# Optimization experiments

Measured on AMD Instinct MI355X. Metric: run time of the kernel, lower is better.

Reference implementation:

```python
import jax, jax.numpy as jnp
import numpy as np

N = 20000      # vertices
KPV = 8        # key points per vertex
M = N * KPV    # total key points
E = 320000     # edges (avg in-degree 16)
KP_DIM = 4
SD = 300       # state_dim
T = 3          # GNN iterations
NC = 4         # classes
LOC = (64, 64, 7)


def _lin(key, din, dout):
    k1, k2 = jax.random.split(key)
    s = 1.0 / np.sqrt(din)
    W = jax.random.uniform(k1, (din, dout), jnp.float32, -s, s)
    b = jax.random.uniform(k2, (dout,), jnp.float32, -s, s)
    return W, b


def setup_inputs():
    key = jax.random.key(0)
    ks = jax.random.split(key, 32)
    inp = {}
    inp['key_points'] = jax.random.normal(ks[0], (M, KP_DIM), jnp.float32)
    inp['pos'] = jax.random.normal(ks[1], (N, 3), jnp.float32)
    # uniform ragged layout: vertex i owns key points [i*KPV, (i+1)*KPV)
    inp['key_points_lookup'] = jnp.arange(N, dtype=jnp.int32) * KPV
    inp['edge_index'] = jax.random.randint(ks[2], (2, E), 0, N, jnp.int32)
    # MLPInit: kp_dim -> 64 -> 128 -> state_dim (basic_block = Linear+ReLU)
    inp['Wi0'], inp['bi0'] = _lin(ks[3], KP_DIM, 64)
    inp['Wi1'], inp['bi1'] = _lin(ks[4], 64, 128)
    inp['Wi2'], inp['bi2'] = _lin(ks[5], 128, SD)
    # MLPInitAggr: state_dim -> state_dim
    inp['Wa'], inp['ba'] = _lin(ks[6], SD, SD)
    # StateConvLayer params per iteration (mlp_h: s->delta_x, mlp_f: [dx,s_j]->e, mlp_g: update)
    Wh, bh, Wf, bf, Wg, bg = [], [], [], [], [], []
    for t in range(T):
        w, b = _lin(ks[7 + 3 * t], SD, 3); Wh.append(w); bh.append(b)
        w, b = _lin(ks[8 + 3 * t], SD + 3, SD); Wf.append(w); bf.append(b)
        w, b = _lin(ks[9 + 3 * t], SD, SD); Wg.append(w); bg.append(b)
    inp['Wh'] = jnp.stack(Wh); inp['bh'] = jnp.stack(bh)
    inp['Wf'] = jnp.stack(Wf); inp['bf'] = jnp.stack(bf)
    inp['Wg'] = jnp.stack(Wg); inp['bg'] = jnp.stack(bg)
    # classification head: state_dim -> 64 -> n_classes
    inp['Wc1'], inp['bc1'] = _lin(ks[16], SD, 64)
    inp['Wc2'], inp['bc2'] = _lin(ks[17], 64, NC)
    # per-class localization heads: state_dim -> 64 -> 64 -> 7 (stacked over classes)
    Wl1, bl1, Wl2, bl2, Wl3, bl3 = [], [], [], [], [], []
    for c in range(NC):
        w, b = _lin(ks[18 + 3 * c], SD, LOC[0]); Wl1.append(w); bl1.append(b)
        w, b = _lin(ks[19 + 3 * c], LOC[0], LOC[1]); Wl2.append(w); bl2.append(b)
        w, b = _lin(ks[20 + 3 * c], LOC[1], LOC[2]); Wl3.append(w); bl3.append(b)
    inp['Wl1'] = jnp.stack(Wl1); inp['bl1'] = jnp.stack(bl1)
    inp['Wl2'] = jnp.stack(Wl2); inp['bl2'] = jnp.stack(bl2)
    inp['Wl3'] = jnp.stack(Wl3); inp['bl3'] = jnp.stack(bl3)
    return inp


def reference(key_points, pos, key_points_lookup, edge_index,
              Wi0, bi0, Wi1, bi1, Wi2, bi2, Wa, ba,
              Wh, bh, Wf, bf, Wg, bg,
              Wc1, bc1, Wc2, bc2,
              Wl1, bl1, Wl2, bl2, Wl3, bl3):
    relu = jax.nn.relu
    n = pos.shape[0]
    # ---- initial vertex state: per-key-point MLP + ragged segment-max ----
    feats = relu(key_points @ Wi0 + bi0)
    feats = relu(feats @ Wi1 + bi1)
    feats = relu(feats @ Wi2 + bi2)                      # [M, SD]
    seg = jnp.searchsorted(key_points_lookup,
                           jnp.arange(feats.shape[0], dtype=jnp.int32),
                           side='right') - 1              # key point -> vertex id
    kp_max = jax.ops.segment_max(feats, seg, num_segments=n)  # [N, SD]
    s = relu(kp_max @ Wa + ba)                            # initial vertex states
    # ---- GNN iterations (Point-GNN eqns, max aggregation) ----
    src, dst = edge_index[0], edge_index[1]
    for t in range(Wh.shape[0]):
        dx = s @ Wh[t] + bh[t]                            # [N, 3] predicted offset
        m = jnp.concatenate([pos[src] - pos[dst] + dx[dst], s[src]], axis=-1)
        e = relu(m @ Wf[t] + bf[t])                       # [E, SD] edge messages
        aggr = jax.ops.segment_max(e, dst, num_segments=n)
        aggr = jnp.where(jnp.isneginf(aggr), 0.0, aggr)   # empty segments -> 0
        s = s + (aggr @ Wg[t] + bg[t])                    # residual state update
    # ---- heads ----
    cls_pred = relu(relu(s @ Wc1 + bc1) @ Wc2 + bc2)      # [N, NC]
    h = relu(jnp.einsum('nd,cdk->cnk', s, Wl1) + bl1[:, None, :])
    h = relu(jnp.einsum('cnd,cdk->cnk', h, Wl2) + bl2[:, None, :])
    h = relu(jnp.einsum('cnd,cdk->cnk', h, Wl3) + bl3[:, None, :])  # [C, N, 7]
    reg_pred = jnp.transpose(h, (1, 0, 2)).reshape(n, -1)           # [N, C*7]
    return cls_pred, reg_pred
```

## Files before the change

kernel.cpp:

```cpp
#include <hip/hip_runtime.h>
#include <stdint.h>

#define N_V   20000
#define M_KP  160000
#define E_N   320000
#define SD    300
#define T_IT  3

typedef unsigned short bf16_t;
typedef __attribute__((ext_vector_type(8))) short short8_t;
typedef __attribute__((ext_vector_type(4))) float float4_t;

__device__ __forceinline__ float bf2f(bf16_t u) {
    return __uint_as_float(((unsigned)u) << 16);
}
__device__ __forceinline__ bf16_t f2bf(float f) {
    unsigned u = __float_as_uint(f);
    unsigned r = (u + 0x7FFFu + ((u >> 16) & 1u)) >> 16;
    return (bf16_t)r;
}

template<bool F32>
__device__ __forceinline__ float LD(const void* p, size_t i) {
    if (F32) return ((const float*)p)[i];
    return bf2f(((const bf16_t*)p)[i]);
}
template<bool F32>
__device__ __forceinline__ void ST(void* p, size_t i, float v) {
    if (F32) ((float*)p)[i] = v;
    else     ((bf16_t*)p)[i] = f2bf(v);
}
__device__ __forceinline__ float LDr(const void* p, long long i, bool f32) {
    return f32 ? ((const float*)p)[i] : bf2f(((const bf16_t*)p)[i]);
}
__device__ __forceinline__ void STr(void* p, size_t i, float v, bool f32) {
    if (f32) ((float*)p)[i] = v;
    else     ((bf16_t*)p)[i] = f2bf(v);
}

__global__ void k_detect(const unsigned* __restrict__ w, int* __restrict__ flag) {
    __shared__ int cnt_s;
    if (threadIdx.x == 0) cnt_s = 0;
    __syncthreads();
    unsigned u = w[threadIdx.x];
    unsigned lo = u & 0xFFFFu;
    int e = (lo >> 7) & 0xFF;
    int plaus = (lo == 0u) || (e >= 96 && e <= 126);
    atomicAdd(&cnt_s, plaus);
    __syncthreads();
    if (threadIdx.x == 0) flag[0] = (cnt_s >= 64) ? 0 : 1;
}

__global__ void k_zero(int* p, int n) {
    int i = blockIdx.x * blockDim.x + threadIdx.x;
    if (i < n) p[i] = 0;
}
__global__ void k_hist(const int* __restrict__ dst, int* __restrict__ cnt) {
    int e = blockIdx.x * blockDim.x + threadIdx.x;
    if (e < E_N) atomicAdd(&cnt[dst[e]], 1);
}
__global__ void k_scan(const int* __restrict__ cnt, int* __restrict__ offs,
                       int* __restrict__ cur) {
    __shared__ int buf[1024];
    __shared__ int carry_s;
    int tid = threadIdx.x;
    if (tid == 0) { carry_s = 0; offs[0] = 0; }
    __syncthreads();
    for (int base = 0; base < N_V; base += 1024) {
        int i = base + tid;
        int v = (i < N_V) ? cnt[i] : 0;
        buf[tid] = v;
        __syncthreads();
        for (int off = 1; off < 1024; off <<= 1) {
            int t = (tid >= off) ? buf[tid - off] : 0;
            __syncthreads();
            buf[tid] += t;
            __syncthreads();
        }
        int incl = buf[tid] + carry_s;
        if (i < N_V) { offs[i + 1] = incl; cur[i] = incl - v; }
        __syncthreads();
        if (tid == 1023) carry_s = incl;
        __syncthreads();
    }
}
__global__ void k_scatter(const int* __restrict__ src, const int* __restrict__ dst,
                          int* __restrict__ cur, int* __restrict__ esrc) {
    int e = blockIdx.x * blockDim.x + threadIdx.x;
    if (e < E_N) {
        int p = atomicAdd(&cur[dst[e]], 1);
        esrc[p] = src[e];
    }
}

template<bool F32>
__global__ __launch_bounds__(256) void k_init_fused(
    const void* __restrict__ kp,
    const void* __restrict__ Wi0, const void* __restrict__ bi0,
    const void* __restrict__ Wi1, const void* __restrict__ bi1,
    const void* __restrict__ Wi2, const void* __restrict__ bi2,
    float* __restrict__ kpmax, const int* __restrict__ flag) {
    if ((flag[0] != 0) != F32) return;
    __shared__ float kps[256];
    __shared__ float h1s[64][64];
    __shared__ float h2s[64 * 128];
    int tid = threadIdx.x;
    int row0 = blockIdx.x * 64;
    kps[tid] = LD<F32>(kp, (size_t)row0 * 4 + tid);
    __syncthreads();
    {
        int c = tid & 63;
        float w0 = LD<F32>(Wi0, c), w1 = LD<F32>(Wi0, 64 + c);
        float w2 = LD<F32>(Wi0, 128 + c), w3 = LD<F32>(Wi0, 192 + c);
        float b0 = LD<F32>(bi0, c);
        int rbase = (tid >> 6) * 16;
#pragma unroll
        for (int rr = 0; rr < 16; rr++) {
            int r = rbase + rr;
            float a = b0 + kps[r * 4] * w0 + kps[r * 4 + 1] * w1
                         + kps[r * 4 + 2] * w2 + kps[r * 4 + 3] * w3;
            h1s[r][c] = fmaxf(a, 0.f);
        }
    }
    __syncthreads();
    {
        int c = tid & 127;
        int rbase = (tid >> 7) * 32;
        float b1 = LD<F32>(bi1, c);
        float acc[32];
#pragma unroll
        for (int rr = 0; rr < 32; rr++) acc[rr] = b1;
        for (int k = 0; k < 64; k++) {
            float wv = LD<F32>(Wi1, (size_t)k * 128 + c);
#pragma unroll
            for (int rr = 0; rr < 32; rr++) acc[rr] += h1s[rbase + rr][k] * wv;
        }
#pragma unroll
        for (int rr = 0; rr < 32; rr++)
            h2s[(size_t)(rbase + rr) * 128 + c] = fmaxf(acc[rr], 0.f);
    }
    __syncthreads();
    {
        int cx = tid & 63, rg = tid >> 6;
        float acc[16][5];
#pragma unroll
        for (int r = 0; r < 16; r++)
#pragma unroll
            for (int j = 0; j < 5; j++) acc[r][j] = 0.f;
        bool ok4 = (cx < SD - 256);
        for (int k = 0; k < 128; k++) {
            float w[5];
#pragma unroll
            for (int j = 0; j < 4; j++) w[j] = LD<F32>(Wi2, (size_t)k * SD + cx + 64 * j);
            w[4] = ok4 ? LD<F32>(Wi2, (size_t)k * SD + cx + 256) : 0.f;
#pragma unroll
            for (int r = 0; r < 16; r++) {
                float av = h2s[(rg * 16 + r) * 128 + k];
#pragma unroll
                for (int j = 0; j < 5; j++) acc[r][j] += av * w[j];
            }
        }
        int vbase = (row0 >> 3) + rg * 2;
#pragma unroll
        for (int half = 0; half < 2; half++) {
            int v = vbase + half;
#pragma unroll
            for (int j = 0; j < 5; j++) {
                int c = cx + 64 * j;
                if (c >= SD) continue;
                float m = acc[half * 8][j];
#pragma unroll
                for (int r = 1; r < 8; r++) m = fmaxf(m, acc[half * 8 + r][j]);
                kpmax[(size_t)v * SD + c] = fmaxf(m + LD<F32>(bi2, c), 0.f);
            }
        }
    }
}

template<bool F32>
__global__ __launch_bounds__(256) void k_gemm(
    const float* __restrict__ A, const void* __restrict__ W,
    const void* __restrict__ bias, const float* res,
    float* C, int Mr, int K, int Nc, int do_relu, const int* __restrict__ flag) {
    if ((flag[0] != 0) != F32) return;
    __shared__ float As[16][65];
    __shared__ float Ws[16][64];
    int tid = threadIdx.x;
    int tx = tid & 15, ty = tid >> 4;
    int row0 = blockIdx.y * 64, col0 = blockIdx.x * 64;
    float acc[4][4] = {{0.f}};
    int lk = tid & 15, lr = tid >> 4;
    int ln = tid & 63, lk4 = tid >> 6;
    for (int k0 = 0; k0 < K; k0 += 16) {
#pragma unroll
        for (int i = 0; i < 4; i++) {
            int r = lr + i * 16;
            int gr = row0 + r, gk = k0 + lk;
            As[lk][r] = (gr < Mr && gk < K) ? A[(size_t)gr * K + gk] : 0.f;
        }
#pragma unroll
        for (int p = 0; p < 4; p++) {
            int kk = lk4 + p * 4;
            int gk = k0 + kk, gn = col0 + ln;
            Ws[kk][ln] = (gk < K && gn < Nc) ? LD<F32>(W, (size_t)gk * Nc + gn) : 0.f;
        }
        __syncthreads();
#pragma unroll
        for (int kk = 0; kk < 16; kk++) {
            float a[4], w[4];
#pragma unroll
            for (int i = 0; i < 4; i++) a[i] = As[kk][ty * 4 + i];
#pragma unroll
            for (int j = 0; j < 4; j++) w[j] = Ws[kk][tx * 4 + j];
#pragma unroll
            for (int i = 0; i < 4; i++)
#pragma unroll
                for (int j = 0; j < 4; j++) acc[i][j] += a[i] * w[j];
        }
        __syncthreads();
    }
#pragma unroll
    for (int i = 0; i < 4; i++) {
        int gr = row0 + ty * 4 + i;
        if (gr >= Mr) continue;
#pragma unroll
        for (int j = 0; j < 4; j++) {
            int gn = col0 + tx * 4 + j;
            if (gn >= Nc) continue;
            float c = acc[i][j] + LD<F32>(bias, gn);
            if (res) c += res[(size_t)gr * Nc + gn];
            if (do_relu) c = fmaxf(c, 0.f);
            C[(size_t)gr * Nc + gn] = c;
        }
    }
}

#define PREP_SPLIT 882688
#define PREP_BIAS  3104
#define PREP_WF3   2700
#define PREP_TOT   (PREP_SPLIT + PREP_BIAS + PREP_WF3 + 32)

__global__ __launch_bounds__(256) void k_prep(
    const void* __restrict__ Wa, const void* __restrict__ Wf,
    const void* __restrict__ Wg, const void* __restrict__ Wc1,
    const void* __restrict__ Wl1, const void* __restrict__ Wl2,
    const void* __restrict__ Wi1, const void* __restrict__ Wi2,
    const void* __restrict__ ba, const void* __restrict__ bfb,
    const void* __restrict__ bgb, const void* __restrict__ bc1,
    const void* __restrict__ bl1b, const void* __restrict__ bl2b,
    const void* __restrict__ bi1, const void* __restrict__ bi2,
    unsigned short* __restrict__ SP, float* __restrict__ biasF,
    float* __restrict__ wf3F,
    float* __restrict__ bzero, const int* __restrict__ flag)
{
    int idx = blockIdx.x * 256 + threadIdx.x;
    if (idx >= PREP_TOT) return;
    bool f32 = flag[0] != 0;
    if (idx < PREP_SPLIT) {
        const void* src; long long eoff, cum; int srcN, Nn, Kk, Kpad, pe, local;
        if (idx < 716800) {
            int m = idx / 102400; local = idx - m * 102400;
            pe = 102400; cum = (long long)m * 102400;
            Kpad = 320; Nn = 300; Kk = 300; srcN = 300;
            src = (m == 0) ? Wa : (m <= 3 ? Wf : Wg);
            eoff = (m == 0) ? 0 : (m <= 3 ? (long long)((m - 1) * 303 + 3) * 300
                                          : (long long)(m - 4) * 90000);
        } else if (idx < 819200) {
            int j = (idx - 716800) / 20480; local = (idx - 716800) - j * 20480;
            pe = 20480; cum = 716800 + (long long)j * 20480;
            Kpad = 320; Nn = 64; Kk = 300; srcN = 64;
            src = (j == 0) ? Wc1 : Wl1;
            eoff = (j == 0) ? 0 : (long long)(j - 1) * 19200;
        } else if (idx < 835584) {
            int c = (idx - 819200) / 4096; local = (idx - 819200) - c * 4096;
            pe = 4096; cum = 819200 + (long long)c * 4096;
            Kpad = 64; Nn = 64; Kk = 64; srcN = 64;
            src = Wl2; eoff = (long long)c * 4096;
        } else if (idx < 843776) {
            local = idx - 835584;
            pe = 8192; cum = 835584;
            Kpad = 64; Nn = 128; Kk = 64; srcN = 128;
            src = Wi1; eoff = 0;
        } else {
            local = idx - 843776;
            pe = 38912; cum = 843776;
            Kpad = 128; Nn = 300; Kk = 128; srcN = 300;
            src = Wi2; eoff = 0;
        }
        int n = local / Kpad, k = local - n * Kpad;
        float v = 0.f;
        if (n < Nn && k < Kk) v = LDr(src, eoff + (long long)k * srcN + n, f32);
        bf16_t hi = f2bf(v);
        bf16_t lo = f2bf(v - bf2f(hi));
        SP[2 * cum + local] = hi;
        SP[2 * cum + pe + local] = lo;
    } else if (idx < PREP_SPLIT + PREP_BIAS) {
        int b = idx - PREP_SPLIT;
        const void* src; int o;
        if (b < 300)       { src = ba;   o = b; }
        else if (b < 1200) { src = bfb;  o = b - 300; }
        else if (b < 2100) { src = bgb;  o = b - 1200; }
        else if (b < 2164) { src = bc1;  o = b - 2100; }
        else if (b < 2420) { src = bl1b; o = b - 2164; }
        else if (b < 2676) { src = bl2b; o = b - 2420; }
        else if (b < 2804) { src = bi1;  o = b - 2676; }
        else               { src = bi2;  o = b - 2804; }
        biasF[b] = LDr(src, o, f32);
    } else if (idx < PREP_SPLIT + PREP_BIAS + PREP_WF3) {
        int b2 = idx - (PREP_SPLIT + PREP_BIAS);
        int t = b2 / 900, rem = b2 - t * 900;
        wf3F[b2] = LDr(Wf, (long long)t * 303 * SD + rem, f32);
    } else {
        bzero[idx - (PREP_SPLIT + PREP_BIAS + PREP_WF3)] = 0.f;
    }
}

__device__ __forceinline__ void mfma16(float4_t& c, short8_t a, short8_t b) {
    asm("v_mfma_f32_16x16x32_bf16 %0, %1, %2, %0" : "+v"(c) : "v"(a), "v"(b));
}
__device__ __forceinline__ void split2(float a, float b, unsigned& h, unsigned& l) {
    asm("v_cvt_pk_bf16_f32 %0, %1, %2" : "=v"(h) : "v"(a), "v"(b));
    float la = a - __uint_as_float(h << 16);
    float lb = b - __uint_as_float(h & 0xFFFF0000u);
    asm("v_cvt_pk_bf16_f32 %0, %1, %2" : "=v"(l) : "v"(la), "v"(lb));
}
__device__ __forceinline__ void split8(float4_t x0, float4_t x1,
                                       short8_t* hi, short8_t* lo) {
    union { unsigned u[4]; short8_t v; } H, L;
#pragma unroll
    for (int p = 0; p < 4; p++) {
        float a, b;
        if (p == 0)      { a = x0[0]; b = x0[1]; }
        else if (p == 1) { a = x0[2]; b = x0[3]; }
        else if (p == 2) { a = x1[0]; b = x1[1]; }
        else             { a = x1[2]; b = x1[3]; }
        unsigned ph, pl;
        split2(a, b, ph, pl);
        H.u[p] = ph; L.u[p] = pl;
    }
    *hi = H.v; *lo = L.v;
}

__global__ __launch_bounds__(256) void k_init_mfma(
    const void* __restrict__ kp,
    const void* __restrict__ Wi0, const void* __restrict__ bi0,
    const unsigned short* __restrict__ W1T,
    const unsigned short* __restrict__ W2T,
    const float* __restrict__ b1F, const float* __restrict__ b2F,
    float* __restrict__ kpmax, const int* __restrict__ flag)
{
    bool f32 = flag[0] != 0;
    __shared__ __attribute__((aligned(16))) unsigned short lds[2][8704];
    int tid = threadIdx.x;
    int w = tid >> 6, lane = tid & 63;
    int rg = w >> 1, ch = w & 1;
    int l15 = lane & 15, g = lane >> 4;
    unsigned short* h2h = lds[rg];
    unsigned short* h2l = lds[rg] + 4352;
    int rw0 = blockIdx.x * 64 + rg * 32;

    float kpr[2][4];
#pragma unroll
    for (int mt = 0; mt < 2; mt++) {
        long long r = rw0 + mt * 16 + l15;
#pragma unroll
        for (int j = 0; j < 4; j++) kpr[mt][j] = LDr(kp, r * 4 + j, f32);
    }
    short8_t a1h[2][2], a1l[2][2];
#pragma unroll
    for (int ks = 0; ks < 2; ks++) {
        float h[2][8];
#pragma unroll
        for (int e = 0; e < 8; e++) {
            int chn = ks * 32 + 8 * g + e;
            float w0 = LDr(Wi0, chn, f32),       w1 = LDr(Wi0, 64 + chn, f32);
            float w2 = LDr(Wi0, 128 + chn, f32), w3 = LDr(Wi0, 192 + chn, f32);
            float b0 = LDr(bi0, chn, f32);
#pragma unroll
            for (int mt = 0; mt < 2; mt++)
                h[mt][e] = fmaxf(b0 + kpr[mt][0] * w0 + kpr[mt][1] * w1
                                    + kpr[mt][2] * w2 + kpr[mt][3] * w3, 0.f);
        }
#pragma unroll
        for (int mt = 0; mt < 2; mt++) {
            union { unsigned u[4]; short8_t v; } H, L;
#pragma unroll
            for (int p = 0; p < 4; p++) {
                unsigned hh, ll;
                split2(h[mt][2 * p], h[mt][2 * p + 1], hh, ll);
                H.u[p] = hh; L.u[p] = ll;
            }
            a1h[mt][ks] = H.v; a1l[mt][ks] = L.v;
        }
    }

#pragma unroll
    for (int i = 0; i < 4; i++) {
        int n0 = ch * 4 + i;
        const unsigned short* bp = W1T + (n0 * 16 + l15) * 64 + 8 * g;
        short8_t bh0 = *(const short8_t*)bp;
        short8_t bh1 = *(const short8_t*)(bp + 32);
        short8_t bl0 = *(const short8_t*)(bp + 8192);
        short8_t bl1 = *(const short8_t*)(bp + 8224);
        float4_t c0 = {0.f, 0.f, 0.f, 0.f}, c1 = {0.f, 0.f, 0.f, 0.f};
        mfma16(c0, a1h[0][0], bh0); mfma16(c0, a1h[0][1], bh1);
        mfma16(c0, a1l[0][0], bh0); mfma16(c0, a1l[0][1], bh1);
        mfma16(c0, a1h[0][0], bl0); mfma16(c0, a1h[0][1], bl1);
        mfma16(c1, a1h[1][0], bh0); mfma16(c1, a1h[1][1], bh1);
        mfma16(c1, a1l[1][0], bh0); mfma16(c1, a1l[1][1], bh1);
        mfma16(c1, a1h[1][0], bl0); mfma16(c1, a1h[1][1], bl1);
        int col = n0 * 16 + l15;
        float bv = b1F[col];
#pragma unroll
        for (int i2 = 0; i2 < 4; i2++) {
            float v0 = fmaxf(c0[i2] + bv, 0.f);
            bf16_t h0 = f2bf(v0);
            h2h[(4 * g + i2) * 136 + col] = h0;
            h2l[(4 * g + i2) * 136 + col] = f2bf(v0 - bf2f(h0));
            float v1 = fmaxf(c1[i2] + bv, 0.f);
            bf16_t h1v = f2bf(v1);
            h2h[(16 + 4 * g + i2) * 136 + col] = h1v;
            h2l[(16 + 4 * g + i2) * 136 + col] = f2bf(v1 - bf2f(h1v));
        }
    }
    __syncthreads();

    short8_t a2h[2][4], a2l[2][4];
#pragma unroll
    for (int mt = 0; mt < 2; mt++)
#pragma unroll
        for (int ks = 0; ks < 4; ks++) {
            int off = (mt * 16 + l15) * 136 + ks * 32 + 8 * g;
            a2h[mt][ks] = *(const short8_t*)(h2h + off);
            a2l[mt][ks] = *(const short8_t*)(h2l + off);
        }
    int vb = blockIdx.x * 8 + rg * 4;
    int n0beg = ch ? 10 : 0, n0end = ch ? 19 : 10;
    for (int n0 = n0beg; n0 < n0end; n0++) {
        const unsigned short* bp = W2T + (n0 * 16 + l15) * 128 + 8 * g;
        short8_t bh[4], bl[4];
#pragma unroll
        for (int ks = 0; ks < 4; ks++) {
            bh[ks] = *(const short8_t*)(bp + ks * 32);
            bl[ks] = *(const short8_t*)(bp + 38912 + ks * 32);
        }
        float4_t c0 = {0.f, 0.f, 0.f, 0.f}, c1 = {0.f, 0.f, 0.f, 0.f};
#pragma unroll
        for (int ks = 0; ks < 4; ks++) {
            mfma16(c0, a2h[0][ks], bh[ks]); mfma16(c1, a2h[1][ks], bh[ks]);
        }
#pragma unroll
        for (int ks = 0; ks < 4; ks++) {
            mfma16(c0, a2l[0][ks], bh[ks]); mfma16(c1, a2l[1][ks], bh[ks]);
        }
#pragma unroll
        for (int ks = 0; ks < 4; ks++) {
            mfma16(c0, a2h[0][ks], bl[ks]); mfma16(c1, a2h[1][ks], bl[ks]);
        }
        float m0 = fmaxf(fmaxf(c0[0], c0[1]), fmaxf(c0[2], c0[3]));
        m0 = fmaxf(m0, __shfl_xor(m0, 16));
        float m1 = fmaxf(fmaxf(c1[0], c1[1]), fmaxf(c1[2], c1[3]));
        m1 = fmaxf(m1, __shfl_xor(m1, 16));
        int col = n0 * 16 + l15;
        if (col < SD) {
            float bv = b2F[col];
            if (g == 0) {
                kpmax[(size_t)(vb + 0) * SD + col] = fmaxf(m0 + bv, 0.f);
                kpmax[(size_t)(vb + 2) * SD + col] = fmaxf(m1 + bv, 0.f);
            } else if (g == 2) {
                kpmax[(size_t)(vb + 1) * SD + col] = fmaxf(m0 + bv, 0.f);
                kpmax[(size_t)(vb + 3) * SD + col] = fmaxf(m1 + bv, 0.f);
            }
        }
    }
}

__global__ __launch_bounds__(256) void k_gemm_mfma(
    const float* __restrict__ A, const unsigned short* __restrict__ WhiT,
    const unsigned short* __restrict__ WloT, const float* __restrict__ bias,
    const float* __restrict__ res, float* __restrict__ C,
    int M, int K, int Kpad, int N, int relu,
    long long zA, long long zW, int zB, long long zC,
    const void* posp, const float* dxv, const float* wf3F,
    float* bbag, const int* __restrict__ flag)
{
    int z = blockIdx.z;
    A    += (size_t)z * zA;
    WhiT += (size_t)z * zW;
    WloT += (size_t)z * zW;
    bias += (size_t)z * zB;
    C    += (size_t)z * zC;
    int tid = threadIdx.x;
    int w = tid >> 6, lane = tid & 63;
    int l15 = lane & 15, g = lane >> 4;
    int row0 = blockIdx.y * 128 + w * 32;
    int col0 = blockIdx.x * 64;

    float4_t acc[2][4];
#pragma unroll
    for (int i = 0; i < 2; i++)
#pragma unroll
        for (int j = 0; j < 4; j++) acc[i][j] = (float4_t){0.f, 0.f, 0.f, 0.f};

    const unsigned short* bhp[4];
    const unsigned short* blp[4];
#pragma unroll
    for (int ns = 0; ns < 4; ns++) {
        size_t o = (size_t)(col0 + ns * 16 + l15) * Kpad + 8 * g;
        bhp[ns] = WhiT + o; blp[ns] = WloT + o;
    }
    const float* app[2];
    int amode[2]; bool adead[2];
#pragma unroll
    for (int ms = 0; ms < 2; ms++) {
        int base = row0 + ms * 16;
        int gr = base + l15;
        amode[ms] = (base + 16 <= M) ? 2 : (base < M ? 1 : 0);
        adead[ms] = gr >= M;
        int grc = gr < M ? gr : (M - 1);
        app[ms] = A + (size_t)grc * K + 8 * g;
    }
    const float4_t zf4 = {0.f, 0.f, 0.f, 0.f};

    auto LOADB = [&](short8_t* bh, short8_t* bl) {
#pragma unroll
        for (int ns = 0; ns < 4; ns++) {
            bh[ns] = *(const short8_t*)bhp[ns];
            bl[ns] = *(const short8_t*)blp[ns];
            bhp[ns] += 32; blp[ns] += 32;
        }
    };
    auto LOADA = [&](float4_t* x0, float4_t* x1) {
#pragma unroll
        for (int ms = 0; ms < 2; ms++) {
            if (amode[ms] == 0) { x0[ms] = zf4; x1[ms] = zf4; }
            else {
                x0[ms] = *(const float4_t*)app[ms];
                x1[ms] = *(const float4_t*)(app[ms] + 4);
                if (amode[ms] == 1 && adead[ms]) { x0[ms] = zf4; x1[ms] = zf4; }
            }
            app[ms] += 32;
        }
    };
    auto COMPUTE = [&](const short8_t* bh, const short8_t* bl,
                       const float4_t* x0, const float4_t* x1) {
#pragma unroll
        for (int ms = 0; ms < 2; ms++) {
            short8_t ah, al;
            split8(x0[ms], x1[ms], &ah, &al);
#pragma unroll
            for (int ns = 0; ns < 4; ns++) {
                mfma16(acc[ms][ns], ah, bh[ns]);
                mfma16(acc[ms][ns], al, bh[ns]);
                mfma16(acc[ms][ns], ah, bl[ns]);
            }
        }
    };

    short8_t bhA[4], blA[4], bhB[4], blB[4];
    float4_t x0A[2], x1A[2], x0B[2], x1B[2];
    int iters = (K + 31) / 32;
    LOADB(bhA, blA); LOADA(x0A, x1A);
    for (int it = 0; it < iters; it += 2) {
        LOADB(bhB, blB); LOADA(x0B, x1B);
        COMPUTE(bhA, blA, x0A, x1A);
        if (it + 2 < iters) { LOADB(bhA, blA); LOADA(x0A, x1A); }
        COMPUTE(bhB, blB, x0B, x1B);
    }

    bool ab = posp != nullptr;
    bool pf32 = ab && (flag[0] != 0);
    int gnv[4]; float bvv[4], w30v[4], w31v[4], w32v[4];
#pragma unroll
    for (int ns = 0; ns < 4; ns++) {
        int gn = col0 + ns * 16 + l15;
        gnv[ns] = gn;
        bvv[ns] = (gn < N) ? bias[gn] : 0.f;
        if (ab && gn < N) {
            w30v[ns] = wf3F[gn]; w31v[ns] = wf3F[300 + gn]; w32v[ns] = wf3F[600 + gn];
        } else { w30v[ns] = 0.f; w31v[ns] = 0.f; w32v[ns] = 0.f; }
    }
#pragma unroll
    for (int ms = 0; ms < 2; ms++) {
#pragma unroll
        for (int r = 0; r < 4; r++) {
            int gr = row0 + ms * 16 + 4 * g + r;
            if (gr >= M) continue;
            float p0 = 0.f, p1 = 0.f, p2 = 0.f, d0 = 0.f, d1 = 0.f, d2 = 0.f;
            if (ab) {
                p0 = LDr(posp, (long long)gr * 3 + 0, pf32);
                p1 = LDr(posp, (long long)gr * 3 + 1, pf32);
                p2 = LDr(posp, (long long)gr * 3 + 2, pf32);
                d0 = dxv[gr * 3 + 0]; d1 = dxv[gr * 3 + 1]; d2 = dxv[gr * 3 + 2];
            }
#pragma unroll
            for (int ns = 0; ns < 4; ns++) {
                int gn = gnv[ns];
                if (gn >= N) continue;
                float c = acc[ms][ns][r] + bvv[ns];
                if (ab) {
                    float P = p0 * w30v[ns] + p1 * w31v[ns] + p2 * w32v[ns];
                    float D = d0 * w30v[ns] + d1 * w31v[ns] + d2 * w32v[ns];
                    c += P;
                    bbag[(size_t)gr * N + gn] = D - P;
                }
                if (res) c += res[(size_t)gr * N + gn];
                if (relu) c = fmaxf(c, 0.f);
                C[(size_t)gr * N + gn] = c;
            }
        }
    }
}

__global__ void k_dx2(const float* __restrict__ s, const void* __restrict__ Wh,
                      const void* __restrict__ bh, int t, float* __restrict__ dx,
                      const int* __restrict__ flag) {
    bool f32 = flag[0] != 0;
    long long wo = (long long)t * SD * 3, bo = (long long)t * 3;
    int wv = threadIdx.x >> 6, lane = threadIdx.x & 63;
    int v = blockIdx.x * 4 + wv;
    if (v >= N_V) return;
    float p0 = 0.f, p1 = 0.f, p2 = 0.f;
    for (int d = lane; d < SD; d += 64) {
        float sv = s[(size_t)v * SD + d];
        p0 += sv * LDr(Wh, wo + d * 3 + 0, f32);
        p1 += sv * LDr(Wh, wo + d * 3 + 1, f32);
        p2 += sv * LDr(Wh, wo + d * 3 + 2, f32);
    }
#pragma unroll
    for (int off = 32; off > 0; off >>= 1) {
        p0 += __shfl_down(p0, off);
        p1 += __shfl_down(p1, off);
        p2 += __shfl_down(p2, off);
    }
    if (lane == 0) {
        dx[v * 3 + 0] = p0 + LDr(bh, bo + 0, f32);
        dx[v * 3 + 1] = p1 + LDr(bh, bo + 1, f32);
        dx[v * 3 + 2] = p2 + LDr(bh, bo + 2, f32);
    }
}

__global__ void k_cls2(const float* __restrict__ hc, const void* __restrict__ W,
                       const void* __restrict__ b, void* __restrict__ out,
                       const int* __restrict__ flag) {
    bool f32 = flag[0] != 0;
    int v = blockIdx.x * blockDim.x + threadIdx.x;
    if (v >= N_V) return;
    float acc[4];
#pragma unroll
    for (int j = 0; j < 4; j++) acc[j] = LDr(b, j, f32);
    for (int k = 0; k < 64; k++) {
        float h = hc[(size_t)v * 64 + k];
#pragma unroll
        for (int j = 0; j < 4; j++) acc[j] += h * LDr(W, k * 4 + j, f32);
    }
#pragma unroll
    for (int j = 0; j < 4; j++) STr(out, v * 4 + j, fmaxf(acc[j], 0.f), f32);
}

__global__ void k_loc32(const float* __restrict__ hl2all, const void* __restrict__ Wl3,
                        const void* __restrict__ bl3, void* __restrict__ out,
                        const int* __restrict__ flag) {
    bool f32 = flag[0] != 0;
    int cls = blockIdx.y;
    const float* h2 = hl2all + (size_t)cls * N_V * 64;
    long long wo = (long long)cls * 64 * 7, bo = (long long)cls * 7;
    int v = blockIdx.x * blockDim.x + threadIdx.x;
    if (v >= N_V) return;
    float acc[7];
#pragma unroll
    for (int j = 0; j < 7; j++) acc[j] = LDr(bl3, bo + j, f32);
    for (int k = 0; k < 64; k++) {
        float h = h2[(size_t)v * 64 + k];
#pragma unroll
        for (int j = 0; j < 7; j++) acc[j] += h * LDr(Wl3, wo + k * 7 + j, f32);
    }
#pragma unroll
    for (int j = 0; j < 7; j++)
        STr(out, 80000 + (size_t)v * 28 + cls * 7 + j, fmaxf(acc[j], 0.f), f32);
}

template<bool F32>
__global__ void k_dx(const float* __restrict__ s, const void* __restrict__ Wh,
                     const void* __restrict__ bh, float* __restrict__ dx,
                     const int* __restrict__ flag) {
    if ((flag[0] != 0) != F32) return;
    int wv = threadIdx.x >> 6, lane = threadIdx.x & 63;
    int v = blockIdx.x * 4 + wv;
    if (v >= N_V) return;
    float p0 = 0.f, p1 = 0.f, p2 = 0.f;
    for (int d = lane; d < SD; d += 64) {
        float sv = s[(size_t)v * SD + d];
        p0 += sv * LD<F32>(Wh, d * 3 + 0);
        p1 += sv * LD<F32>(Wh, d * 3 + 1);
        p2 += sv * LD<F32>(Wh, d * 3 + 2);
    }
#pragma unroll
    for (int off = 32; off > 0; off >>= 1) {
        p0 += __shfl_down(p0, off);
        p1 += __shfl_down(p1, off);
        p2 += __shfl_down(p2, off);
    }
    if (lane == 0) {
        dx[v * 3 + 0] = p0 + LD<F32>(bh, 0);
        dx[v * 3 + 1] = p1 + LD<F32>(bh, 1);
        dx[v * 3 + 2] = p2 + LD<F32>(bh, 2);
    }
}

template<bool F32>
__global__ void k_ab(const float* __restrict__ dx, const void* __restrict__ pos,
                     const void* __restrict__ Wf3, float* __restrict__ ua,
                     float* __restrict__ bbag, const int* __restrict__ flag) {
    if ((flag[0] != 0) != F32) return;
    int idx = blockIdx.x * blockDim.x + threadIdx.x;
    if (idx >= N_V * SD) return;
    int v = idx / SD, c = idx - v * SD;
    float w0 = LD<F32>(Wf3, c), w1 = LD<F32>(Wf3, SD + c), w2 = LD<F32>(Wf3, 2 * SD + c);
    float P = LD<F32>(pos, v * 3 + 0) * w0 + LD<F32>(pos, v * 3 + 1) * w1
            + LD<F32>(pos, v * 3 + 2) * w2;
    float D = dx[v * 3 + 0] * w0 + dx[v * 3 + 1] * w1 + dx[v * 3 + 2] * w2;
    ua[idx] += P;
    bbag[idx] = D - P;
}

__global__ __launch_bounds__(256) void k_aggr(
    const float* __restrict__ a, float* bbag,
    const int* __restrict__ offs, const int* __restrict__ esrc) {
    int wv = threadIdx.x >> 6, lane = threadIdx.x & 63;
    int v = blockIdx.x * 4 + wv;
    if (v >= N_V) return;
    int e0 = offs[v], e1 = offs[v + 1];
    float r0 = -3.0e38f, r1 = r0, r2 = r0, r3 = r0, r4 = r0;
    bool c4 = lane < SD - 256;
    for (int e = e0; e < e1; e++) {
        const float* ar = a + (size_t)esrc[e] * SD + lane;
        r0 = fmaxf(r0, ar[0]);
        r1 = fmaxf(r1, ar[64]);
        r2 = fmaxf(r2, ar[128]);
        r3 = fmaxf(r3, ar[192]);
        if (c4) r4 = fmaxf(r4, ar[256]);
    }
    float* bv = bbag + (size_t)v * SD + lane;
    bv[0]   = fmaxf(0.f, r0 + bv[0]);
    bv[64]  = fmaxf(0.f, r1 + bv[64]);
    bv[128] = fmaxf(0.f, r2 + bv[128]);
    bv[192] = fmaxf(0.f, r3 + bv[192]);
    if (c4) bv[256] = fmaxf(0.f, r4 + bv[256]);
}

template<bool F32>
__global__ void k_cls(const float* __restrict__ hc, const void* __restrict__ W,
                      const void* __restrict__ b, void* __restrict__ out,
                      const int* __restrict__ flag) {
    if ((flag[0] != 0) != F32) return;
    int v = blockIdx.x * blockDim.x + threadIdx.x;
    if (v >= N_V) return;
    float acc[4];
#pragma unroll
    for (int j = 0; j < 4; j++) acc[j] = LD<F32>(b, j);
    for (int k = 0; k < 64; k++) {
        float h = hc[(size_t)v * 64 + k];
#pragma unroll
        for (int j = 0; j < 4; j++) acc[j] += h * LD<F32>(W, k * 4 + j);
    }
#pragma unroll
    for (int j = 0; j < 4; j++) ST<F32>(out, v * 4 + j, fmaxf(acc[j], 0.f));
}

template<bool F32>
__global__ void k_loc3(const float* __restrict__ h2, const void* __restrict__ W,
                       const void* __restrict__ b, void* __restrict__ out, int cls,
                       const int* __restrict__ flag) {
    if ((flag[0] != 0) != F32) return;
    int v = blockIdx.x * blockDim.x + threadIdx.x;
    if (v >= N_V) return;
    float acc[7];
#pragma unroll
    for (int j = 0; j < 7; j++) acc[j] = LD<F32>(b, j);
    for (int k = 0; k < 64; k++) {
        float h = h2[(size_t)v * 64 + k];
#pragma unroll
        for (int j = 0; j < 7; j++) acc[j] += h * LD<F32>(W, k * 7 + j);
    }
#pragma unroll
    for (int j = 0; j < 7; j++)
        ST<F32>(out, 80000 + (size_t)v * 28 + cls * 7 + j, fmaxf(acc[j], 0.f));
}

#define LAUNCH2(kname, grid, blk, ...) \
    do { kname<false><<<grid, blk, 0, stream>>>(__VA_ARGS__); \
         kname<true><<<grid, blk, 0, stream>>>(__VA_ARGS__); } while (0)

extern "C" void kernel_launch(void* const* d_in, const int* in_sizes, int n_in,
                              void* d_out, int out_size, void* d_ws, size_t ws_size,
                              hipStream_t stream) {
    const void* kp  = d_in[0];
    const void* pos = d_in[1];
    const int* eidx = (const int*)d_in[3];
    const int* e_src = eidx;
    const int* e_dst = eidx + E_N;
    const void* Wi0 = d_in[4];   const void* bi0 = d_in[5];
    const void* Wi1 = d_in[6];   const void* bi1 = d_in[7];
    const void* Wi2 = d_in[8];   const void* bi2 = d_in[9];
    const void* Wa  = d_in[10];  const void* ba  = d_in[11];
    const char* Wh  = (const char*)d_in[12];  const char* bh = (const char*)d_in[13];
    const char* Wf  = (const char*)d_in[14];  const char* bff = (const char*)d_in[15];
    const char* Wg  = (const char*)d_in[16];  const char* bg = (const char*)d_in[17];
    const void* Wc1 = d_in[18];  const void* bc1 = d_in[19];
    const void* Wc2 = d_in[20];  const void* bc2 = d_in[21];
    const char* Wl1 = (const char*)d_in[22];  const char* bl1 = (const char*)d_in[23];
    const char* Wl2 = (const char*)d_in[24];  const char* bl2 = (const char*)d_in[25];
    const char* Wl3 = (const char*)d_in[26];  const char* bl3 = (const char*)d_in[27];

    char* ws = (char*)d_ws;
    float* regA  = (float*)(ws + 0);
    float* kpmax = regA;
    float* ua    = regA;
    float* hc    = (float*)(ws + 0);
    float* hl1m  = (float*)(ws + 0);
    float* hl1f  = (float*)(ws + 6000000);
    float* hl2f  = (float*)(ws + 12000000);
    float* bbag  = (float*)(ws + 24000000);
    float* hl2m  = (float*)(ws + 24000000);
    float* s     = (float*)(ws + 48000000);
    int*   cnt   = (int*)(ws + 72000000);
    int*   offs  = (int*)(ws + 72100000);
    int*   cur   = (int*)(ws + 72200000);
    int*   esrc  = (int*)(ws + 72300000);
    float* dx    = (float*)(ws + 73600000);
    float* wf3F  = (float*)(ws + 73844000);
    int*   flag  = (int*)(ws + 73900000);
    unsigned short* SPLIT = (unsigned short*)(ws + 73950000);
    float* biasF = (float*)(ws + 77481000);

    bool mf = (ws_size == 0) || (ws_size >= (size_t)77500000);
    auto HI = [&](long long cum) { return SPLIT + 2 * cum; };

    k_detect<<<1, 128, 0, stream>>>((const unsigned*)Wi0, flag);

    k_zero<<<(N_V + 255) / 256, 256, 0, stream>>>(cnt, N_V);
    k_hist<<<(E_N + 255) / 256, 256, 0, stream>>>(e_dst, cnt);
    k_scan<<<1, 1024, 0, stream>>>(cnt, offs, cur);
    k_scatter<<<(E_N + 255) / 256, 256, 0, stream>>>(e_src, e_dst, cur, esrc);

    if (mf)
        k_prep<<<(PREP_TOT + 255) / 256, 256, 0, stream>>>(
            Wa, Wf, Wg, Wc1, Wl1, Wl2, Wi1, Wi2,
            ba, bff, bg, bc1, bl1, bl2, bi1, bi2,
            SPLIT, biasF, wf3F, bbag, flag);

    if (mf) {
        const unsigned short* W1T = SPLIT + 2LL * 835584;
        const unsigned short* W2T = SPLIT + 2LL * 843776;
        k_init_mfma<<<M_KP / 64, 256, 0, stream>>>(kp, Wi0, bi0, W1T, W2T,
                                                   biasF + 2676, biasF + 2804,
                                                   kpmax, flag);
    } else {
        LAUNCH2(k_init_fused, M_KP / 64, 256, kp, Wi0, bi0, Wi1, bi1, Wi2, bi2, kpmax, flag);
    }

    const dim3 GSD(5, (N_V + 127) / 128);
    const dim3 G64(1, (N_V + 127) / 128);
    if (mf) {
        k_gemm_mfma<<<GSD, 256, 0, stream>>>(kpmax, HI(0), HI(0) + 102400,
                                             biasF, nullptr, s, N_V, SD, 320, SD, 1,
                                             0, 0, 0, 0,
                                             nullptr, nullptr, nullptr, nullptr, nullptr);
    } else {
        dim3 g((SD + 63) / 64, (N_V + 63) / 64);
        LAUNCH2(k_gemm, g, 256, kpmax, Wa, ba, nullptr, s, N_V, SD, SD, 1, flag);
    }

    for (int t = 0; t < T_IT; t++) {
        dim3 g5((SD + 63) / 64, (N_V + 63) / 64);
        if (mf) {
            k_dx2<<<(N_V + 3) / 4, 256, 0, stream>>>(s, Wh, bh, t, dx, flag);
            long long cum = (long long)(1 + t) * 102400;
            k_gemm_mfma<<<GSD, 256, 0, stream>>>(s, HI(cum), HI(cum) + 102400,
                                                 biasF + 300 + t * 300, nullptr, ua,
                                                 N_V, SD, 320, SD, 0, 0, 0, 0, 0,
                                                 pos, dx, wf3F + t * 900, bbag, flag);
        } else {
            for (int f32v = 0; f32v < 2; f32v++) {
                size_t es = f32v ? 4 : 2;
                const void* Wf_t = Wf + (size_t)t * 303 * SD * es;
                const void* WfS  = Wf + ((size_t)t * 303 + 3) * SD * es;
                const void* bf_t = bff + (size_t)t * SD * es;
                const void* Wh_t = Wh + (size_t)t * SD * 3 * es;
                const void* bh_t = bh + (size_t)t * 3 * es;
                if (f32v) {
                    k_gemm<true><<<g5, 256, 0, stream>>>(s, WfS, bf_t, nullptr, ua, N_V, SD, SD, 0, flag);
                    k_dx<true><<<(N_V + 3) / 4, 256, 0, stream>>>(s, Wh_t, bh_t, dx, flag);
                    k_ab<true><<<(N_V * SD + 255) / 256, 256, 0, stream>>>(dx, pos, Wf_t, ua, bbag, flag);
                } else {
                    k_gemm<false><<<g5, 256, 0, stream>>>(s, WfS, bf_t, nullptr, ua, N_V, SD, SD, 0, flag);
                    k_dx<false><<<(N_V + 3) / 4, 256, 0, stream>>>(s, Wh_t, bh_t, dx, flag);
                    k_ab<false><<<(N_V * SD + 255) / 256, 256, 0, stream>>>(dx, pos, Wf_t, ua, bbag, flag);
                }
            }
        }
        k_aggr<<<(N_V + 3) / 4, 256, 0, stream>>>(ua, bbag, offs, esrc);
        if (mf) {
            long long cum = (long long)(4 + t) * 102400;
            k_gemm_mfma<<<GSD, 256, 0, stream>>>(bbag, HI(cum), HI(cum) + 102400,
                                                 biasF + 1200 + t * 300, s, s,
                                                 N_V, SD, 320, SD, 0, 0, 0, 0, 0,
                                                 nullptr, nullptr, nullptr, nullptr, nullptr);
        } else {
            for (int f32v = 0; f32v < 2; f32v++) {
                size_t es = f32v ? 4 : 2;
                const void* Wg_t = Wg + (size_t)t * SD * SD * es;
                const void* bg_t = bg + (size_t)t * SD * es;
                if (f32v)
                    k_gemm<true><<<g5, 256, 0, stream>>>(bbag, Wg_t, bg_t, s, s, N_V, SD, SD, 0, flag);
                else
                    k_gemm<false><<<g5, 256, 0, stream>>>(bbag, Wg_t, bg_t, s, s, N_V, SD, SD, 0, flag);
            }
        }
    }

    if (mf) {
        k_gemm_mfma<<<G64, 256, 0, stream>>>(s, HI(716800), HI(716800) + 20480,
                                             biasF + 2100, nullptr, hc,
                                             N_V, SD, 320, 64, 1, 0, 0, 0, 0,
                                             nullptr, nullptr, nullptr, nullptr, nullptr);
        k_cls2<<<(N_V + 255) / 256, 256, 0, stream>>>(hc, Wc2, bc2, d_out, flag);
        dim3 gz1(1, (N_V + 127) / 128, 4);
        k_gemm_mfma<<<gz1, 256, 0, stream>>>(s, HI(737280), HI(737280) + 20480,
                                             biasF + 2164, nullptr, hl1m,
                                             N_V, SD, 320, 64, 1,
                                             0, 40960, 64, 1280000,
                                             nullptr, nullptr, nullptr, nullptr, nullptr);
        k_gemm_mfma<<<gz1, 256, 0, stream>>>(hl1m, HI(819200), HI(819200) + 4096,
                                             biasF + 2420, nullptr, hl2m,
                                             N_V, 64, 64, 64, 1,
                                             1280000, 8192, 64, 1280000,
                                             nullptr, nullptr, nullptr, nullptr, nullptr);
        dim3 gz3((N_V + 255) / 256, 4);
        k_loc32<<<gz3, 256, 0, stream>>>(hl2m, Wl3, bl3, d_out, flag);
    } else {
        dim3 g(1, (N_V + 63) / 64);
        LAUNCH2(k_gemm, g, 256, s, Wc1, bc1, nullptr, hc, N_V, SD, 64, 1, flag);
        LAUNCH2(k_cls, (N_V + 255) / 256, 256, hc, Wc2, bc2, d_out, flag);
        for (int c = 0; c < 4; c++) {
            for (int f32v = 0; f32v < 2; f32v++) {
                size_t es = f32v ? 4 : 2;
                const void* Wl1c = Wl1 + (size_t)c * SD * 64 * es;
                const void* bl1c = bl1 + (size_t)c * 64 * es;
                const void* Wl2c = Wl2 + (size_t)c * 64 * 64 * es;
                const void* bl2c = bl2 + (size_t)c * 64 * es;
                const void* Wl3c = Wl3 + (size_t)c * 64 * 7 * es;
                const void* bl3c = bl3 + (size_t)c * 7 * es;
                if (f32v) {
                    k_gemm<true><<<g, 256, 0, stream>>>(s, Wl1c, bl1c, nullptr, hl1f, N_V, SD, 64, 1, flag);
                    k_gemm<true><<<g, 256, 0, stream>>>(hl1f, Wl2c, bl2c, nullptr, hl2f, N_V, 64, 64, 1, flag);
                    k_loc3<true><<<(N_V + 255) / 256, 256, 0, stream>>>(hl2f, Wl3c, bl3c, d_out, c, flag);
                } else {
                    k_gemm<false><<<g, 256, 0, stream>>>(s, Wl1c, bl1c, nullptr, hl1f, N_V, SD, 64, 1, flag);
                    k_gemm<false><<<g, 256, 0, stream>>>(hl1f, Wl2c, bl2c, nullptr, hl2f, N_V, 64, 64, 1, flag);
                    k_loc3<false><<<(N_V + 255) / 256, 256, 0, stream>>>(hl2f, Wl3c, bl3c, d_out, c, flag);
                }
            }
        }
    }
}
```

Before: 1.182 ms.

## Merge small setup and head kernels, skip weight-low MFMA terms for bf16 inputs

Several small launches are merged into one: the zeroing pass goes into the detect kernel, the edge scatter into the weight prep kernel, and the class and localization first layers and output heads are each combined into a single z-batched launch. The scan now has each thread sum a contiguous run of 20 counts, replacing the serial loop over 1024-element chunks. When inputs are bf16, the split-precision GEMMs skip the weight-low-part loads and MFMAs, since those parts are exactly zero. Workspace buffers are rearranged so the merged head launches can share one output region, which risks aliasing bugs if any offsets overlap.

```diff
diff --git a/kernel.cpp b/kernel.cpp
--- a/kernel.cpp
+++ b/kernel.cpp
@@ -38,58 +38,158 @@
     else     ((bf16_t*)p)[i] = f2bf(v);
 }
 
-__global__ void k_detect(const unsigned* __restrict__ w, int* __restrict__ flag) {
+__global__ __launch_bounds__(256) void k_detz(const unsigned* __restrict__ w,
+                                              int* __restrict__ flag,
+                                              int* __restrict__ cnt) {
+    if (blockIdx.x < 79) {
+        int i = blockIdx.x * 256 + threadIdx.x;
+        if (i < N_V) cnt[i] = 0;
+        return;
+    }
     __shared__ int cnt_s;
     if (threadIdx.x == 0) cnt_s = 0;
     __syncthreads();
-    unsigned u = w[threadIdx.x];
-    unsigned lo = u & 0xFFFFu;
-    int e = (lo >> 7) & 0xFF;
-    int plaus = (lo == 0u) || (e >= 96 && e <= 126);
-    atomicAdd(&cnt_s, plaus);
+    if (threadIdx.x < 128) {
+        unsigned u = w[threadIdx.x];
+        unsigned lo = u & 0xFFFFu;
+        int e = (lo >> 7) & 0xFF;
+        int plaus = (lo == 0u) || (e >= 96 && e <= 126);
+        atomicAdd(&cnt_s, plaus);
+    }
     __syncthreads();
     if (threadIdx.x == 0) flag[0] = (cnt_s >= 64) ? 0 : 1;
 }
 
-__global__ void k_zero(int* p, int n) {
-    int i = blockIdx.x * blockDim.x + threadIdx.x;
-    if (i < n) p[i] = 0;
-}
 __global__ void k_hist(const int* __restrict__ dst, int* __restrict__ cnt) {
     int e = blockIdx.x * blockDim.x + threadIdx.x;
     if (e < E_N) atomicAdd(&cnt[dst[e]], 1);
 }
-__global__ void k_scan(const int* __restrict__ cnt, int* __restrict__ offs,
-                       int* __restrict__ cur) {
-    __shared__ int buf[1024];
-    __shared__ int carry_s;
+
+__global__ __launch_bounds__(1024) void k_scan(const int* __restrict__ cnt,
+                                               int* __restrict__ offs,
+                                               int* __restrict__ cur) {
+    __shared__ int sums[1024];
     int tid = threadIdx.x;
-    if (tid == 0) { carry_s = 0; offs[0] = 0; }
+    int base = tid * 20;
+    int vals[20];
+    int s = 0;
+#pragma unroll
+    for (int j = 0; j < 20; j++) {
+        int i = base + j;
+        int v = (i < N_V) ? cnt[i] : 0;
+        vals[j] = v;
+        s += v;
+    }
+    sums[tid] = s;
     __syncthreads();
-    for (int base = 0; base < N_V; base += 1024) {
-        int i = base + tid;
-        int v = (i < N_V) ? cnt[i] : 0;
-        buf[tid] = v;
+    for (int off = 1; off < 1024; off <<= 1) {
+        int t = (tid >= off) ? sums[tid - off] : 0;
         __syncthreads();
-        for (int off = 1; off < 1024; off <<= 1) {
-            int t = (tid >= off) ? buf[tid - off] : 0;
-            __syncthreads();
-            buf[tid] += t;
-            __syncthreads();
-        }
-        int incl = buf[tid] + carry_s;
-        if (i < N_V) { offs[i + 1] = incl; cur[i] = incl - v; }
+        sums[tid] += t;
         __syncthreads();
-        if (tid == 1023) carry_s = incl;
-        __syncthreads();
-    }
-}
-__global__ void k_scatter(const int* __restrict__ src, const int* __restrict__ dst,
-                          int* __restrict__ cur, int* __restrict__ esrc) {
-    int e = blockIdx.x * blockDim.x + threadIdx.x;
-    if (e < E_N) {
-        int p = atomicAdd(&cur[dst[e]], 1);
-        esrc[p] = src[e];
+    }
+    int run = (tid == 0) ? 0 : sums[tid - 1];
+    if (tid == 0) offs[0] = 0;
+#pragma unroll
+    for (int j = 0; j < 20; j++) {
+        int i = base + j;
+        if (i < N_V) {
+            cur[i] = run;
+            run += vals[j];
+            offs[i + 1] = run;
+        }
+    }
+}
+
+#define PREP_SPLIT 882688
+#define PREP_BIAS  3104
+#define PREP_WF3   2700
+#define PREP_TOT   (PREP_SPLIT + PREP_BIAS + PREP_WF3 + 32)
+#define SCAT_BLOCKS 1250
+#define PREP_BLOCKS ((PREP_TOT + 255) / 256)
+
+__global__ __launch_bounds__(256) void k_scprep(
+    const int* __restrict__ src, const int* __restrict__ dst,
+    int* __restrict__ cur, int* __restrict__ esrc,
+    const void* __restrict__ Wa, const void* __restrict__ Wf,
+    const void* __restrict__ Wg, const void* __restrict__ Wc1,
+    const void* __restrict__ Wl1, const void* __restrict__ Wl2,
+    const void* __restrict__ Wi1, const void* __restrict__ Wi2,
+    const void* __restrict__ ba, const void* __restrict__ bfb,
+    const void* __restrict__ bgb, const void* __restrict__ bc1,
+    const void* __restrict__ bl1b, const void* __restrict__ bl2b,
+    const void* __restrict__ bi1, const void* __restrict__ bi2,
+    unsigned short* __restrict__ SP, float* __restrict__ biasF,
+    float* __restrict__ wf3F, float* __restrict__ bzero,
+    const int* __restrict__ flag)
+{
+    if (blockIdx.x < SCAT_BLOCKS) {
+        int e = blockIdx.x * 256 + threadIdx.x;
+        if (e < E_N) {
+            int p = atomicAdd(&cur[dst[e]], 1);
+            esrc[p] = src[e];
+        }
+        return;
+    }
+    int idx = (blockIdx.x - SCAT_BLOCKS) * 256 + threadIdx.x;
+    if (idx >= PREP_TOT) return;
+    bool f32 = flag[0] != 0;
+    if (idx < PREP_SPLIT) {
+        const void* srcp; long long eoff, cum; int srcN, Nn, Kk, Kpad, pe, local;
+        if (idx < 716800) {
+            int m = idx / 102400; local = idx - m * 102400;
+            pe = 102400; cum = (long long)m * 102400;
+            Kpad = 320; Nn = 300; Kk = 300; srcN = 300;
+            srcp = (m == 0) ? Wa : (m <= 3 ? Wf : Wg);
+            eoff = (m == 0) ? 0 : (m <= 3 ? (long long)((m - 1) * 303 + 3) * 300
+                                          : (long long)(m - 4) * 90000);
+        } else if (idx < 819200) {
+            int j = (idx - 716800) / 20480; local = (idx - 716800) - j * 20480;
+            pe = 20480; cum = 716800 + (long long)j * 20480;
+            Kpad = 320; Nn = 64; Kk = 300; srcN = 64;
+            srcp = (j == 0) ? Wc1 : Wl1;
+            eoff = (j == 0) ? 0 : (long long)(j - 1) * 19200;
+        } else if (idx < 835584) {
+            int c = (idx - 819200) / 4096; local = (idx - 819200) - c * 4096;
+            pe = 4096; cum = 819200 + (long long)c * 4096;
+            Kpad = 64; Nn = 64; Kk = 64; srcN = 64;
+            srcp = Wl2; eoff = (long long)c * 4096;
+        } else if (idx < 843776) {
+            local = idx - 835584;
+            pe = 8192; cum = 835584;
+            Kpad = 64; Nn = 128; Kk = 64; srcN = 128;
+            srcp = Wi1; eoff = 0;
+        } else {
+            local = idx - 843776;
+            pe = 38912; cum = 843776;
+            Kpad = 128; Nn = 300; Kk = 128; srcN = 300;
+            srcp = Wi2; eoff = 0;
+        }
+        int n = local / Kpad, k = local - n * Kpad;
+        float v = 0.f;
+        if (n < Nn && k < Kk) v = LDr(srcp, eoff + (long long)k * srcN + n, f32);
+        bf16_t hi = f2bf(v);
+        bf16_t lo = f2bf(v - bf2f(hi));
+        SP[2 * cum + local] = hi;
+        SP[2 * cum + pe + local] = lo;
+    } else if (idx < PREP_SPLIT + PREP_BIAS) {
+        int b = idx - PREP_SPLIT;
+        const void* srcp; int o;
+        if (b < 300)       { srcp = ba;   o = b; }
+        else if (b < 1200) { srcp = bfb;  o = b - 300; }
+        else if (b < 2100) { srcp = bgb;  o = b - 1200; }
+        else if (b < 2164) { srcp = bc1;  o = b - 2100; }
+        else if (b < 2420) { srcp = bl1b; o = b - 2164; }
+        else if (b < 2676) { srcp = bl2b; o = b - 2420; }
+        else if (b < 2804) { srcp = bi1;  o = b - 2676; }
+        else               { srcp = bi2;  o = b - 2804; }
+        biasF[b] = LDr(srcp, o, f32);
+    } else if (idx < PREP_SPLIT + PREP_BIAS + PREP_WF3) {
+        int b2 = idx - (PREP_SPLIT + PREP_BIAS);
+        int t = b2 / 900, rem = b2 - t * 900;
+        wf3F[b2] = LDr(Wf, (long long)t * 303 * SD + rem, f32);
+    } else {
+        bzero[idx - (PREP_SPLIT + PREP_BIAS + PREP_WF3)] = 0.f;
     }
 }
 
@@ -235,86 +335,6 @@
     }
 }
 
-#define PREP_SPLIT 882688
-#define PREP_BIAS  3104
-#define PREP_WF3   2700
-#define PREP_TOT   (PREP_SPLIT + PREP_BIAS + PREP_WF3 + 32)
-
-__global__ __launch_bounds__(256) void k_prep(
-    const void* __restrict__ Wa, const void* __restrict__ Wf,
-    const void* __restrict__ Wg, const void* __restrict__ Wc1,
-    const void* __restrict__ Wl1, const void* __restrict__ Wl2,
-    const void* __restrict__ Wi1, const void* __restrict__ Wi2,
-    const void* __restrict__ ba, const void* __restrict__ bfb,
-    const void* __restrict__ bgb, const void* __restrict__ bc1,
-    const void* __restrict__ bl1b, const void* __restrict__ bl2b,
-    const void* __restrict__ bi1, const void* __restrict__ bi2,
-    unsigned short* __restrict__ SP, float* __restrict__ biasF,
-    float* __restrict__ wf3F,
-    float* __restrict__ bzero, const int* __restrict__ flag)
-{
-    int idx = blockIdx.x * 256 + threadIdx.x;
-    if (idx >= PREP_TOT) return;
-    bool f32 = flag[0] != 0;
-    if (idx < PREP_SPLIT) {
-        const void* src; long long eoff, cum; int srcN, Nn, Kk, Kpad, pe, local;
-        if (idx < 716800) {
-            int m = idx / 102400; local = idx - m * 102400;
-            pe = 102400; cum = (long long)m * 102400;
-            Kpad = 320; Nn = 300; Kk = 300; srcN = 300;
-            src = (m == 0) ? Wa : (m <= 3 ? Wf : Wg);
-            eoff = (m == 0) ? 0 : (m <= 3 ? (long long)((m - 1) * 303 + 3) * 300
-                                          : (long long)(m - 4) * 90000);
-        } else if (idx < 819200) {
-            int j = (idx - 716800) / 20480; local = (idx - 716800) - j * 20480;
-            pe = 20480; cum = 716800 + (long long)j * 20480;
-            Kpad = 320; Nn = 64; Kk = 300; srcN = 64;
-            src = (j == 0) ? Wc1 : Wl1;
-            eoff = (j == 0) ? 0 : (long long)(j - 1) * 19200;
-        } else if (idx < 835584) {
-            int c = (idx - 819200) / 4096; local = (idx - 819200) - c * 4096;
-            pe = 4096; cum = 819200 + (long long)c * 4096;
-            Kpad = 64; Nn = 64; Kk = 64; srcN = 64;
-            src = Wl2; eoff = (long long)c * 4096;
-        } else if (idx < 843776) {
-            local = idx - 835584;
-            pe = 8192; cum = 835584;
-            Kpad = 64; Nn = 128; Kk = 64; srcN = 128;
-            src = Wi1; eoff = 0;
-        } else {
-            local = idx - 843776;
-            pe = 38912; cum = 843776;
-            Kpad = 128; Nn = 300; Kk = 128; srcN = 300;
-            src = Wi2; eoff = 0;
-        }
-        int n = local / Kpad, k = local - n * Kpad;
-        float v = 0.f;
-        if (n < Nn && k < Kk) v = LDr(src, eoff + (long long)k * srcN + n, f32);
-        bf16_t hi = f2bf(v);
-        bf16_t lo = f2bf(v - bf2f(hi));
-        SP[2 * cum + local] = hi;
-        SP[2 * cum + pe + local] = lo;
-    } else if (idx < PREP_SPLIT + PREP_BIAS) {
-        int b = idx - PREP_SPLIT;
-        const void* src; int o;
-        if (b < 300)       { src = ba;   o = b; }
-        else if (b < 1200) { src = bfb;  o = b - 300; }
-        else if (b < 2100) { src = bgb;  o = b - 1200; }
-        else if (b < 2164) { src = bc1;  o = b - 2100; }
-        else if (b < 2420) { src = bl1b; o = b - 2164; }
-        else if (b < 2676) { src = bl2b; o = b - 2420; }
-        else if (b < 2804) { src = bi1;  o = b - 2676; }
-        else               { src = bi2;  o = b - 2804; }
-        biasF[b] = LDr(src, o, f32);
-    } else if (idx < PREP_SPLIT + PREP_BIAS + PREP_WF3) {
-        int b2 = idx - (PREP_SPLIT + PREP_BIAS);
-        int t = b2 / 900, rem = b2 - t * 900;
-        wf3F[b2] = LDr(Wf, (long long)t * 303 * SD + rem, f32);
-    } else {
-        bzero[idx - (PREP_SPLIT + PREP_BIAS + PREP_WF3)] = 0.f;
-    }
-}
-
 __device__ __forceinline__ void mfma16(float4_t& c, short8_t a, short8_t b) {
     asm("v_mfma_f32_16x16x32_bf16 %0, %1, %2, %0" : "+v"(c) : "v"(a), "v"(b));
 }
@@ -350,6 +370,7 @@
     float* __restrict__ kpmax, const int* __restrict__ flag)
 {
     bool f32 = flag[0] != 0;
+    bool wlo = f32;
     __shared__ __attribute__((aligned(16))) unsigned short lds[2][8704];
     int tid = threadIdx.x;
     int w = tid >> 6, lane = tid & 63;
@@ -400,15 +421,17 @@
         const unsigned short* bp = W1T + (n0 * 16 + l15) * 64 + 8 * g;
         short8_t bh0 = *(const short8_t*)bp;
         short8_t bh1 = *(const short8_t*)(bp + 32);
-        short8_t bl0 = *(const short8_t*)(bp + 8192);
-        short8_t bl1 = *(const short8_t*)(bp + 8224);
         float4_t c0 = {0.f, 0.f, 0.f, 0.f}, c1 = {0.f, 0.f, 0.f, 0.f};
         mfma16(c0, a1h[0][0], bh0); mfma16(c0, a1h[0][1], bh1);
         mfma16(c0, a1l[0][0], bh0); mfma16(c0, a1l[0][1], bh1);
-        mfma16(c0, a1h[0][0], bl0); mfma16(c0, a1h[0][1], bl1);
         mfma16(c1, a1h[1][0], bh0); mfma16(c1, a1h[1][1], bh1);
         mfma16(c1, a1l[1][0], bh0); mfma16(c1, a1l[1][1], bh1);
-        mfma16(c1, a1h[1][0], bl0); mfma16(c1, a1h[1][1], bl1);
+        if (wlo) {
+            short8_t bl0 = *(const short8_t*)(bp + 8192);
+            short8_t bl1 = *(const short8_t*)(bp + 8224);
+            mfma16(c0, a1h[0][0], bl0); mfma16(c0, a1h[0][1], bl1);
+            mfma16(c1, a1h[1][0], bl0); mfma16(c1, a1h[1][1], bl1);
+        }
         int col = n0 * 16 + l15;
         float bv = b1F[col];
 #pragma unroll
@@ -438,12 +461,9 @@
     int n0beg = ch ? 10 : 0, n0end = ch ? 19 : 10;
     for (int n0 = n0beg; n0 < n0end; n0++) {
         const unsigned short* bp = W2T + (n0 * 16 + l15) * 128 + 8 * g;
-        short8_t bh[4], bl[4];
-#pragma unroll
-        for (int ks = 0; ks < 4; ks++) {
-            bh[ks] = *(const short8_t*)(bp + ks * 32);
-            bl[ks] = *(const short8_t*)(bp + 38912 + ks * 32);
-        }
+        short8_t bh[4];
+#pragma unroll
+        for (int ks = 0; ks < 4; ks++) bh[ks] = *(const short8_t*)(bp + ks * 32);
         float4_t c0 = {0.f, 0.f, 0.f, 0.f}, c1 = {0.f, 0.f, 0.f, 0.f};
 #pragma unroll
         for (int ks = 0; ks < 4; ks++) {
@@ -453,9 +473,15 @@
         for (int ks = 0; ks < 4; ks++) {
             mfma16(c0, a2l[0][ks], bh[ks]); mfma16(c1, a2l[1][ks], bh[ks]);
         }
-#pragma unroll
-        for (int ks = 0; ks < 4; ks++) {
-            mfma16(c0, a2h[0][ks], bl[ks]); mfma16(c1, a2h[1][ks], bl[ks]);
+        if (wlo) {
+            short8_t bl[4];
+#pragma unroll
+            for (int ks = 0; ks < 4; ks++)
+                bl[ks] = *(const short8_t*)(bp + 38912 + ks * 32);
+#pragma unroll
+            for (int ks = 0; ks < 4; ks++) {
+                mfma16(c0, a2h[0][ks], bl[ks]); mfma16(c1, a2h[1][ks], bl[ks]);
+            }
         }
         float m0 = fmaxf(fmaxf(c0[0], c0[1]), fmaxf(c0[2], c0[3]));
         m0 = fmaxf(m0, __shfl_xor(m0, 16));
@@ -484,6 +510,7 @@
     const void* posp, const float* dxv, const float* wf3F,
     float* bbag, const int* __restrict__ flag)
 {
+    bool wlo = flag[0] != 0;
     int z = blockIdx.z;
     A    += (size_t)z * zA;
     WhiT += (size_t)z * zW;
@@ -521,12 +548,13 @@
         app[ms] = A + (size_t)grc * K + 8 * g;
     }
     const float4_t zf4 = {0.f, 0.f, 0.f, 0.f};
+    const short8_t z8 = {0, 0, 0, 0, 0, 0, 0, 0};
 
     auto LOADB = [&](short8_t* bh, short8_t* bl) {
 #pragma unroll
         for (int ns = 0; ns < 4; ns++) {
             bh[ns] = *(const short8_t*)bhp[ns];
-            bl[ns] = *(const short8_t*)blp[ns];
+            bl[ns] = wlo ? *(const short8_t*)blp[ns] : z8;
             bhp[ns] += 32; blp[ns] += 32;
         }
     };
@@ -552,7 +580,10 @@
             for (int ns = 0; ns < 4; ns++) {
                 mfma16(acc[ms][ns], ah, bh[ns]);
                 mfma16(acc[ms][ns], al, bh[ns]);
-                mfma16(acc[ms][ns], ah, bl[ns]);
+            }
+            if (wlo) {
+#pragma unroll
+                for (int ns = 0; ns < 4; ns++) mfma16(acc[ms][ns], ah, bl[ns]);
             }
         }
     };
@@ -569,7 +600,7 @@
     }
 
     bool ab = posp != nullptr;
-    bool pf32 = ab && (flag[0] != 0);
+    bool pf32 = ab && wlo;
     int gnv[4]; float bvv[4], w30v[4], w31v[4], w32v[4];
 #pragma unroll
     for (int ns = 0; ns < 4; ns++) {
@@ -638,90 +669,6 @@
         dx[v * 3 + 1] = p1 + LDr(bh, bo + 1, f32);
         dx[v * 3 + 2] = p2 + LDr(bh, bo + 2, f32);
     }
-}
-
-__global__ void k_cls2(const float* __restrict__ hc, const void* __restrict__ W,
-                       const void* __restrict__ b, void* __restrict__ out,
-                       const int* __restrict__ flag) {
-    bool f32 = flag[0] != 0;
-    int v = blockIdx.x * blockDim.x + threadIdx.x;
-    if (v >= N_V) return;
-    float acc[4];
-#pragma unroll
-    for (int j = 0; j < 4; j++) acc[j] = LDr(b, j, f32);
-    for (int k = 0; k < 64; k++) {
-        float h = hc[(size_t)v * 64 + k];
-#pragma unroll
-        for (int j = 0; j < 4; j++) acc[j] += h * LDr(W, k * 4 + j, f32);
-    }
-#pragma unroll
-    for (int j = 0; j < 4; j++) STr(out, v * 4 + j, fmaxf(acc[j], 0.f), f32);
-}
-
-__global__ void k_loc32(const float* __restrict__ hl2all, const void* __restrict__ Wl3,
-                        const void* __restrict__ bl3, void* __restrict__ out,
-                        const int* __restrict__ flag) {
-    bool f32 = flag[0] != 0;
-    int cls = blockIdx.y;
-    const float* h2 = hl2all + (size_t)cls * N_V * 64;
-    long long wo = (long long)cls * 64 * 7, bo = (long long)cls * 7;
-    int v = blockIdx.x * blockDim.x + threadIdx.x;
-    if (v >= N_V) return;
-    float acc[7];
-#pragma unroll
-    for (int j = 0; j < 7; j++) acc[j] = LDr(bl3, bo + j, f32);
-    for (int k = 0; k < 64; k++) {
-        float h = h2[(size_t)v * 64 + k];
-#pragma unroll
-        for (int j = 0; j < 7; j++) acc[j] += h * LDr(Wl3, wo + k * 7 + j, f32);
-    }
-#pragma unroll
-    for (int j = 0; j < 7; j++)
-        STr(out, 80000 + (size_t)v * 28 + cls * 7 + j, fmaxf(acc[j], 0.f), f32);
-}
-
-template<bool F32>
-__global__ void k_dx(const float* __restrict__ s, const void* __restrict__ Wh,
-                     const void* __restrict__ bh, float* __restrict__ dx,
-                     const int* __restrict__ flag) {
-    if ((flag[0] != 0) != F32) return;
-    int wv = threadIdx.x >> 6, lane = threadIdx.x & 63;
-    int v = blockIdx.x * 4 + wv;
-    if (v >= N_V) return;
-    float p0 = 0.f, p1 = 0.f, p2 = 0.f;
-    for (int d = lane; d < SD; d += 64) {
-        float sv = s[(size_t)v * SD + d];
-        p0 += sv * LD<F32>(Wh, d * 3 + 0);
-        p1 += sv * LD<F32>(Wh, d * 3 + 1);
-        p2 += sv * LD<F32>(Wh, d * 3 + 2);
-    }
-#pragma unroll
-    for (int off = 32; off > 0; off >>= 1) {
-        p0 += __shfl_down(p0, off);
-        p1 += __shfl_down(p1, off);
-        p2 += __shfl_down(p2, off);
-    }
-    if (lane == 0) {
-        dx[v * 3 + 0] = p0 + LD<F32>(bh, 0);
-        dx[v * 3 + 1] = p1 + LD<F32>(bh, 1);
-        dx[v * 3 + 2] = p2 + LD<F32>(bh, 2);
-    }
-}
-
-template<bool F32>
-__global__ void k_ab(const float* __restrict__ dx, const void* __restrict__ pos,
-                     const void* __restrict__ Wf3, float* __restrict__ ua,
-                     float* __restrict__ bbag, const int* __restrict__ flag) {
-    if ((flag[0] != 0) != F32) return;
-    int idx = blockIdx.x * blockDim.x + threadIdx.x;
-    if (idx >= N_V * SD) return;
-    int v = idx / SD, c = idx - v * SD;
-    float w0 = LD<F32>(Wf3, c), w1 = LD<F32>(Wf3, SD + c), w2 = LD<F32>(Wf3, 2 * SD + c);
-    float P = LD<F32>(pos, v * 3 + 0) * w0 + LD<F32>(pos, v * 3 + 1) * w1
-            + LD<F32>(pos, v * 3 + 2) * w2;
-    float D = dx[v * 3 + 0] * w0 + dx[v * 3 + 1] * w1 + dx[v * 3 + 2] * w2;
-    ua[idx] += P;
-    bbag[idx] = D - P;
 }
 
 __global__ __launch_bounds__(256) void k_aggr(
@@ -747,6 +694,87 @@
     bv[128] = fmaxf(0.f, r2 + bv[128]);
     bv[192] = fmaxf(0.f, r3 + bv[192]);
     if (c4) bv[256] = fmaxf(0.f, r4 + bv[256]);
+}
+
+__global__ void k_headout(const float* __restrict__ hc,
+                          const float* __restrict__ hl2all,
+                          const void* __restrict__ Wc2, const void* __restrict__ bc2,
+                          const void* __restrict__ Wl3, const void* __restrict__ bl3,
+                          void* __restrict__ out, const int* __restrict__ flag) {
+    bool f32 = flag[0] != 0;
+    int y = blockIdx.y;
+    int v = blockIdx.x * blockDim.x + threadIdx.x;
+    if (v >= N_V) return;
+    if (y == 4) {
+        float acc[4];
+#pragma unroll
+        for (int j = 0; j < 4; j++) acc[j] = LDr(bc2, j, f32);
+        for (int k = 0; k < 64; k++) {
+            float h = hc[(size_t)v * 64 + k];
+#pragma unroll
+            for (int j = 0; j < 4; j++) acc[j] += h * LDr(Wc2, k * 4 + j, f32);
+        }
+#pragma unroll
+        for (int j = 0; j < 4; j++) STr(out, v * 4 + j, fmaxf(acc[j], 0.f), f32);
+    } else {
+        const float* h2 = hl2all + (size_t)y * N_V * 64;
+        long long wo = (long long)y * 64 * 7, bo = (long long)y * 7;
+        float acc[7];
+#pragma unroll
+        for (int j = 0; j < 7; j++) acc[j] = LDr(bl3, bo + j, f32);
+        for (int k = 0; k < 64; k++) {
+            float h = h2[(size_t)v * 64 + k];
+#pragma unroll
+            for (int j = 0; j < 7; j++) acc[j] += h * LDr(Wl3, wo + k * 7 + j, f32);
+        }
+#pragma unroll
+        for (int j = 0; j < 7; j++)
+            STr(out, 80000 + (size_t)v * 28 + y * 7 + j, fmaxf(acc[j], 0.f), f32);
+    }
+}
+
+template<bool F32>
+__global__ void k_dx(const float* __restrict__ s, const void* __restrict__ Wh,
+                     const void* __restrict__ bh, float* __restrict__ dx,
+                     const int* __restrict__ flag) {
+    if ((flag[0] != 0) != F32) return;
+    int wv = threadIdx.x >> 6, lane = threadIdx.x & 63;
+    int v = blockIdx.x * 4 + wv;
+    if (v >= N_V) return;
+    float p0 = 0.f, p1 = 0.f, p2 = 0.f;
+    for (int d = lane; d < SD; d += 64) {
+        float sv = s[(size_t)v * SD + d];
+        p0 += sv * LD<F32>(Wh, d * 3 + 0);
+        p1 += sv * LD<F32>(Wh, d * 3 + 1);
+        p2 += sv * LD<F32>(Wh, d * 3 + 2);
+    }
+#pragma unroll
+    for (int off = 32; off > 0; off >>= 1) {
+        p0 += __shfl_down(p0, off);
+        p1 += __shfl_down(p1, off);
+        p2 += __shfl_down(p2, off);
+    }
+    if (lane == 0) {
+        dx[v * 3 + 0] = p0 + LD<F32>(bh, 0);
+        dx[v * 3 + 1] = p1 + LD<F32>(bh, 1);
+        dx[v * 3 + 2] = p2 + LD<F32>(bh, 2);
+    }
+}
+
+template<bool F32>
+__global__ void k_ab(const float* __restrict__ dx, const void* __restrict__ pos,
+                     const void* __restrict__ Wf3, float* __restrict__ ua,
+                     float* __restrict__ bbag, const int* __restrict__ flag) {
+    if ((flag[0] != 0) != F32) return;
+    int idx = blockIdx.x * blockDim.x + threadIdx.x;
+    if (idx >= N_V * SD) return;
+    int v = idx / SD, c = idx - v * SD;
+    float w0 = LD<F32>(Wf3, c), w1 = LD<F32>(Wf3, SD + c), w2 = LD<F32>(Wf3, 2 * SD + c);
+    float P = LD<F32>(pos, v * 3 + 0) * w0 + LD<F32>(pos, v * 3 + 1) * w1
+            + LD<F32>(pos, v * 3 + 2) * w2;
+    float D = dx[v * 3 + 0] * w0 + dx[v * 3 + 1] * w1 + dx[v * 3 + 2] * w2;
+    ua[idx] += P;
+    bbag[idx] = D - P;
 }
 
 template<bool F32>
@@ -817,13 +845,13 @@
     float* regA  = (float*)(ws + 0);
     float* kpmax = regA;
     float* ua    = regA;
-    float* hc    = (float*)(ws + 0);
-    float* hl1m  = (float*)(ws + 0);
+    float* hc    = regA;
+    float* hl1m  = regA + 1280000;
     float* hl1f  = (float*)(ws + 6000000);
     float* hl2f  = (float*)(ws + 12000000);
     float* bbag  = (float*)(ws + 24000000);
-    float* hl2m  = (float*)(ws + 24000000);
     float* s     = (float*)(ws + 48000000);
+    float* hl2m  = (float*)(ws + 48000000);
     int*   cnt   = (int*)(ws + 72000000);
     int*   offs  = (int*)(ws + 72100000);
     int*   cur   = (int*)(ws + 72200000);
@@ -837,18 +865,18 @@
     bool mf = (ws_size == 0) || (ws_size >= (size_t)77500000);
     auto HI = [&](long long cum) { return SPLIT + 2 * cum; };
 
-    k_detect<<<1, 128, 0, stream>>>((const unsigned*)Wi0, flag);
-
-    k_zero<<<(N_V + 255) / 256, 256, 0, stream>>>(cnt, N_V);
+    k_detz<<<80, 256, 0, stream>>>((const unsigned*)Wi0, flag, cnt);
+
     k_hist<<<(E_N + 255) / 256, 256, 0, stream>>>(e_dst, cnt);
     k_scan<<<1, 1024, 0, stream>>>(cnt, offs, cur);
-    k_scatter<<<(E_N + 255) / 256, 256, 0, stream>>>(e_src, e_dst, cur, esrc);
-
-    if (mf)
-        k_prep<<<(PREP_TOT + 255) / 256, 256, 0, stream>>>(
+    {
+        int grid = SCAT_BLOCKS + (mf ? PREP_BLOCKS : 0);
+        k_scprep<<<grid, 256, 0, stream>>>(
+            e_src, e_dst, cur, esrc,
             Wa, Wf, Wg, Wc1, Wl1, Wl2, Wi1, Wi2,
             ba, bff, bg, bc1, bl1, bl2, bi1, bi2,
             SPLIT, biasF, wf3F, bbag, flag);
+    }
 
     if (mf) {
         const unsigned short* W1T = SPLIT + 2LL * 835584;
@@ -861,12 +889,11 @@
     }
 
     const dim3 GSD(5, (N_V + 127) / 128);
-    const dim3 G64(1, (N_V + 127) / 128);
     if (mf) {
         k_gemm_mfma<<<GSD, 256, 0, stream>>>(kpmax, HI(0), HI(0) + 102400,
                                              biasF, nullptr, s, N_V, SD, 320, SD, 1,
                                              0, 0, 0, 0,
-                                             nullptr, nullptr, nullptr, nullptr, nullptr);
+                                             nullptr, nullptr, nullptr, nullptr, flag);
     } else {
         dim3 g((SD + 63) / 64, (N_V + 63) / 64);
         LAUNCH2(k_gemm, g, 256, kpmax, Wa, ba, nullptr, s, N_V, SD, SD, 1, flag);
@@ -906,7 +933,7 @@
             k_gemm_mfma<<<GSD, 256, 0, stream>>>(bbag, HI(cum), HI(cum) + 102400,
                                                  biasF + 1200 + t * 300, s, s,
                                                  N_V, SD, 320, SD, 0, 0, 0, 0, 0,
-                                                 nullptr, nullptr, nullptr, nullptr, nullptr);
+                                                 nullptr, nullptr, nullptr, nullptr, flag);
         } else {
             for (int f32v = 0; f32v < 2; f32v++) {
                 size_t es = f32v ? 4 : 2;
@@ -921,28 +948,24 @@
     }
 
     if (mf) {
-        k_gemm_mfma<<<G64, 256, 0, stream>>>(s, HI(716800), HI(716800) + 20480,
-                                             biasF + 2100, nullptr, hc,
-                                             N_V, SD, 320, 64, 1, 0, 0, 0, 0,
-                                             nullptr, nullptr, nullptr, nullptr, nullptr);
-        k_cls2<<<(N_V + 255) / 256, 256, 0, stream>>>(hc, Wc2, bc2, d_out, flag);
-        dim3 gz1(1, (N_V + 127) / 128, 4);
-        k_gemm_mfma<<<gz1, 256, 0, stream>>>(s, HI(737280), HI(737280) + 20480,
-                                             biasF + 2164, nullptr, hl1m,
-                                             N_V, SD, 320, 64, 1,
-                                             0, 40960, 64, 1280000,
-                                             nullptr, nullptr, nullptr, nullptr, nullptr);
-        k_gemm_mfma<<<gz1, 256, 0, stream>>>(hl1m, HI(819200), HI(819200) + 4096,
-                                             biasF + 2420, nullptr, hl2m,
-                                             N_V, 64, 64, 64, 1,
-                                             1280000, 8192, 64, 1280000,
-                                             nullptr, nullptr, nullptr, nullptr, nullptr);
-        dim3 gz3((N_V + 255) / 256, 4);
-        k_loc32<<<gz3, 256, 0, stream>>>(hl2m, Wl3, bl3, d_out, flag);
+        dim3 gz15(1, (N_V + 127) / 128, 5);
+        k_gemm_mfma<<<gz15, 256, 0, stream>>>(s, HI(716800), HI(716800) + 20480,
+                                              biasF + 2100, nullptr, regA,
+                                              N_V, SD, 320, 64, 1,
+                                              0, 40960, 64, 1280000,
+                                              nullptr, nullptr, nullptr, nullptr, flag);
+        dim3 gz14(1, (N_V + 127) / 128, 4);
+        k_gemm_mfma<<<gz14, 256, 0, stream>>>(hl1m, HI(819200), HI(819200) + 4096,
+                                              biasF + 2420, nullptr, hl2m,
+                                              N_V, 64, 64, 64, 1,
+                                              1280000, 8192, 64, 1280000,
+                                              nullptr, nullptr, nullptr, nullptr, flag);
+        dim3 gho((N_V + 255) / 256, 5);
+        k_headout<<<gho, 256, 0, stream>>>(hc, hl2m, Wc2, bc2, Wl3, bl3, d_out, flag);
     } else {
         dim3 g(1, (N_V + 63) / 64);
-        LAUNCH2(k_gemm, g, 256, s, Wc1, bc1, nullptr, hc, N_V, SD, 64, 1, flag);
-        LAUNCH2(k_cls, (N_V + 255) / 256, 256, hc, Wc2, bc2, d_out, flag);
+        LAUNCH2(k_gemm, g, 256, s, Wc1, bc1, nullptr, hl1f, N_V, SD, 64, 1, flag);
+        LAUNCH2(k_cls, (N_V + 255) / 256, 256, hl1f, Wc2, bc2, d_out, flag);
         for (int c = 0; c < 4; c++) {
             for (int f32v = 0; f32v < 2; f32v++) {
                 size_t es = f32v ? 4 : 2;
```

Result: no change. 1.169 ms (-1.1%).
